# Performance work log

Measured on AMD Instinct MI355X. Metric: run time of the kernel, lower is better.

Reference implementation:

```python
import jax, jax.numpy as jnp
import numpy as np

D1, D2, DK, NH = 1024, 1024, 1024, 1
B, S = 4, 2048


def setup_inputs() -> dict:
    key = jax.random.key(0)
    ks = jax.random.split(key, 12)
    scale1 = 1.0 / np.sqrt(D1)
    scale2 = 1.0 / np.sqrt(D2)
    scalek = 1.0 / np.sqrt(DK)
    return {
        "x": jax.random.normal(ks[0], (B, S, D1), dtype=jnp.float32),
        "y": jax.random.normal(ks[1], (B, S, D2), dtype=jnp.float32),
        "adj": jax.random.uniform(ks[2], (B, S, S), dtype=jnp.float32),
        "Wq": jax.random.uniform(ks[3], (D1, DK), jnp.float32, -scale1, scale1),
        "bq": jax.random.uniform(ks[4], (DK,), jnp.float32, -scale1, scale1),
        "Wk": jax.random.uniform(ks[5], (D2, DK), jnp.float32, -scale2, scale2),
        "bk": jax.random.uniform(ks[6], (DK,), jnp.float32, -scale2, scale2),
        "Wv": jax.random.uniform(ks[7], (D2, DK), jnp.float32, -scale2, scale2),
        "bv": jax.random.uniform(ks[8], (DK,), jnp.float32, -scale2, scale2),
        "Wo": jax.random.uniform(ks[9], (DK, D2), jnp.float32, -scalek, scalek),
        "bo": jax.random.uniform(ks[10], (D2,), jnp.float32, -scalek, scalek),
    }


def reference(x, y, adj, Wq, bq, Wk, bk, Wv, bv, Wo, bo):
    # Single-head (n_heads=1) cross-attention with additive adjacency bias.
    dk_head = DK // NH
    norm = 1.0 / np.sqrt(DK)
    Q = (x @ Wq + bq).reshape(NH, B, S, dk_head)   # [h,b,s,d]
    K = (y @ Wk + bk).reshape(NH, B, S, dk_head)
    V = (y @ Wv + bv).reshape(NH, B, S, dk_head)
    att = jnp.einsum('hbsd,hbtd->hbst', Q, K) * norm  # [h,b,s,t]
    att = jax.nn.softmax(att + adj, axis=-1)          # adj [b,s,t] broadcasts over h
    tmp = jnp.einsum('hbst,hbtd->hbsd', att, V).reshape(B, S, -1)  # [b,s,dk]
    out = (tmp @ Wo + bo).reshape(-1, S, D2)
    return out
```

## Files before the change

### kernel.cpp

```cpp
#include <hip/hip_runtime.h>
#include <stdint.h>

typedef unsigned short u16;
using bf16x8 = __attribute__((ext_vector_type(8))) short;
using f32x4  = __attribute__((ext_vector_type(4))) float;

#define NORM 0.03125f

enum { M_PROJ = 0, M_EXP = 1, M_PV = 2, M_OUT = 3 };

__device__ __forceinline__ u16 f2bf(float f) {
  uint32_t u = __float_as_uint(f);
  return (u16)((u + 0x7FFFu + ((u >> 16) & 1u)) >> 16);
}

__device__ __forceinline__ void gload_lds16(const void* g, void* lds) {
  __builtin_amdgcn_global_load_lds(
      (const __attribute__((address_space(1))) uint32_t*)g,
      (__attribute__((address_space(3))) uint32_t*)lds, 16, 0, 0);
}

__global__ void k_cvt(const float* __restrict__ in, u16* __restrict__ out, int n4) {
  int i = blockIdx.x * blockDim.x + threadIdx.x;
  if (i >= n4) return;
  float4 v = ((const float4*)in)[i];
  uint32_t lo = f2bf(v.x) | ((uint32_t)f2bf(v.y) << 16);
  uint32_t hi = f2bf(v.z) | ((uint32_t)f2bf(v.w) << 16);
  ((uint2*)out)[i] = make_uint2(lo, hi);
}

__global__ void k_tc(const float* __restrict__ W0, const float* __restrict__ W1,
                     const float* __restrict__ W2, const float* __restrict__ W3,
                     u16* __restrict__ dst) {
  __shared__ float t[64][65];
  const float* W = blockIdx.z == 0 ? W0 : blockIdx.z == 1 ? W1 : blockIdx.z == 2 ? W2 : W3;
  u16* WT = dst + (size_t)blockIdx.z * (1024 * 1024);
  int c0 = blockIdx.x * 64, r0 = blockIdx.y * 64;
  int c = threadIdx.x & 63, q = threadIdx.x >> 6;
  for (int r = q; r < 64; r += 4) t[r][c] = W[(size_t)(r0 + r) * 1024 + c0 + c];
  __syncthreads();
  for (int r = q; r < 64; r += 4) WT[(size_t)(c0 + r) * 1024 + r0 + c] = f2bf(t[c][r]);
}

struct GArgs {
  const u16* A; const u16* B; int lda, ldb; long long bstrideB; int K;
  const float* bias; const float* adj; float* dpart; const float* dpart_r;
  void* C; int ldc;
  const u16* A1; const u16* B1; const u16* B2;
  const float* bias1; const float* bias2; void* C1; void* C2;
};

template <int MODE>
__global__ __launch_bounds__(512, 2) void gemm8(GArgs g) {
  __shared__ __align__(16) u16 sm[65536];

  const int tid = threadIdx.x, lane = tid & 63, wid = tid >> 6;
  const int wm = wid >> 2, wn = wid & 3;
  const int m0 = blockIdx.x * 256;
  const int n0 = blockIdx.y * 256;
  const int b = m0 >> 11;

  const u16* A = g.A; const u16* B = g.B;
  const float* bias = g.bias; void* C = g.C;
  int zmode = 0;
  if constexpr (MODE == M_PROJ) {
    int z = blockIdx.z; zmode = z;
    if (z == 1) { A = g.A1; B = g.B1; bias = g.bias1; C = g.C1; }
    else if (z == 2) { A = g.A1; B = g.B2; bias = g.bias2; C = g.C2; }
  }
  const int lda = g.lda, ldb = g.ldb, K = g.K, NT = K >> 6;
  const u16* Bp = B + (size_t)b * g.bstrideB;

  f32x4 acc[8][4] = {};

  auto stage = [&](const u16* src, int ld, int r0, int kc, int dst_u16) {
#pragma unroll
    for (int j = 0; j < 2; ++j) {
      int row = wid * 16 + j * 128 + (lane >> 2);
      int cb = (lane & 3) * 16;
      int csw = cb ^ ((row & 8) << 2);
      gload_lds16(src + (size_t)(r0 + row) * ld + kc + (csw >> 1),
                  (void*)&sm[dst_u16 + wid * 512 + j * 4096]);
    }
  };
  auto stA = [&](int v, int kh) {
    stage(A, lda, m0, v * 64 + kh * 32, (v & 1) * 32768 + kh * 8192);
  };
  auto stB = [&](int v, int kh) {
    stage(Bp, ldb, n0, v * 64 + kh * 32, (v & 1) * 32768 + 16384 + kh * 8192);
  };

  stA(0, 0); stB(0, 0); stA(0, 1); stB(0, 1);
  stA(1, 0); stB(1, 0);
  __builtin_amdgcn_sched_barrier(0);
  asm volatile("s_waitcnt vmcnt(8)" ::: "memory");
  __builtin_amdgcn_sched_barrier(0);
  __builtin_amdgcn_s_barrier();
  __builtin_amdgcn_sched_barrier(0);

  const int cb = (lane >> 4) * 16;
  for (int u = 0; u < NT; ++u) {
    const int base = (u & 1) * 32768;
#pragma unroll
    for (int ph = 0; ph < 4; ++ph) {
      const int h = ph & 1, kh = ph >> 1;
      bf16x8 af[4], bfr[4];
#pragma unroll
      for (int m = 0; m < 4; ++m) {
        int row = wm * 128 + h * 64 + m * 16 + (lane & 15);
        af[m] = *(const bf16x8*)__builtin_assume_aligned(
            &sm[base + kh * 8192 + row * 32 + ((cb ^ ((row & 8) << 2)) >> 1)], 16);
      }
#pragma unroll
      for (int n = 0; n < 4; ++n) {
        int row = wn * 64 + n * 16 + (lane & 15);
        bfr[n] = *(const bf16x8*)__builtin_assume_aligned(
            &sm[base + 16384 + kh * 8192 + row * 32 + ((cb ^ ((row & 8) << 2)) >> 1)], 16);
      }
      if (ph == 0) {
        if (u + 1 < NT) stA(u + 1, 1);
      } else if (ph == 1) {
        if (u + 1 < NT) stB(u + 1, 1);
        __builtin_amdgcn_sched_barrier(0);
        if (u + 1 < NT) asm volatile("s_waitcnt vmcnt(4)" ::: "memory");
        else            asm volatile("s_waitcnt vmcnt(0)" ::: "memory");
        __builtin_amdgcn_sched_barrier(0);
      } else if (ph == 2) {
        if (u + 2 < NT) stA(u + 2, 0);
      } else {
        if (u + 2 < NT) stB(u + 2, 0);
      }
      __builtin_amdgcn_s_barrier();
      __builtin_amdgcn_sched_barrier(0);
      __builtin_amdgcn_s_setprio(1);
#pragma unroll
      for (int m = 0; m < 4; ++m)
#pragma unroll
        for (int n = 0; n < 4; ++n)
          acc[h * 4 + m][n] = __builtin_amdgcn_mfma_f32_16x16x32_bf16(
              af[m], bfr[n], acc[h * 4 + m][n], 0, 0, 0);
      __builtin_amdgcn_s_setprio(0);
      __builtin_amdgcn_sched_barrier(0);
      asm volatile("s_waitcnt lgkmcnt(0)" ::: "memory");
      __builtin_amdgcn_sched_barrier(0);
      __builtin_amdgcn_s_barrier();
      __builtin_amdgcn_sched_barrier(0);
    }
  }

  const int lr = lane >> 4, lc = lane & 15;

  if constexpr (MODE == M_PROJ) {
    if (zmode < 2) {
      u16* Cc = (u16*)C;
#pragma unroll
      for (int i = 0; i < 8; ++i) {
        int rowo = (i >> 2) * 64 + (i & 3) * 16;
#pragma unroll
        for (int n = 0; n < 4; ++n) {
          int gcol = n0 + wn * 64 + n * 16 + lc;
          float bv = bias[gcol];
#pragma unroll
          for (int r = 0; r < 4; ++r) {
            int grow = m0 + wm * 128 + rowo + lr * 4 + r;
            Cc[(size_t)grow * g.ldc + gcol] = f2bf(acc[i][n][r] + bv);
          }
        }
      }
    } else {
      u16* Cc = (u16*)C;
#pragma unroll
      for (int i = 0; i < 8; ++i) {
        int rowo = (i >> 2) * 64 + (i & 3) * 16;
        int grow0 = m0 + wm * 128 + rowo + lr * 4;
        int t0 = grow0 & 2047;
#pragma unroll
        for (int n = 0; n < 4; ++n) {
          int gcol = n0 + wn * 64 + n * 16 + lc;
          float bv = bias[gcol];
          ushort4 pk = make_ushort4(f2bf(acc[i][n][0] + bv), f2bf(acc[i][n][1] + bv),
                                    f2bf(acc[i][n][2] + bv), f2bf(acc[i][n][3] + bv));
          *(ushort4*)&Cc[((size_t)b * 1024 + gcol) * 2048 + t0] = pk;
        }
      }
    }
  } else if constexpr (MODE == M_EXP) {
    u16* Cc = (u16*)C;
    float esum[8][4];
#pragma unroll
    for (int i = 0; i < 8; ++i)
#pragma unroll
      for (int r = 0; r < 4; ++r) esum[i][r] = 0.f;
#pragma unroll
    for (int i = 0; i < 8; ++i) {
      int rowo = (i >> 2) * 64 + (i & 3) * 16;
#pragma unroll
      for (int n = 0; n < 4; ++n) {
        int gcol = n0 + wn * 64 + n * 16 + lc;
#pragma unroll
        for (int r = 0; r < 4; ++r) {
          int grow = m0 + wm * 128 + rowo + lr * 4 + r;
          float z = acc[i][n][r] * NORM + g.adj[(size_t)grow * 2048 + gcol];
          float e = __expf(z);
          Cc[(size_t)grow * 2048 + gcol] = f2bf(e);
          esum[i][r] += e;
        }
      }
    }
    int pidx = blockIdx.y * 4 + wn;
#pragma unroll
    for (int i = 0; i < 8; ++i) {
      int rowo = (i >> 2) * 64 + (i & 3) * 16;
#pragma unroll
      for (int r = 0; r < 4; ++r) {
        float s = esum[i][r];
        s += __shfl_xor(s, 1); s += __shfl_xor(s, 2);
        s += __shfl_xor(s, 4); s += __shfl_xor(s, 8);
        if (lc == 0)
          g.dpart[(size_t)pidx * 8192 + m0 + wm * 128 + rowo + lr * 4 + r] = s;
      }
    }
  } else if constexpr (MODE == M_PV) {
    __shared__ float dinv[256];
    if (tid < 256) {
      float s = 0.f;
#pragma unroll
      for (int t = 0; t < 32; ++t) s += g.dpart_r[(size_t)t * 8192 + m0 + tid];
      dinv[tid] = 1.0f / s;
    }
    __syncthreads();
    u16* Cc = (u16*)C;
#pragma unroll
    for (int i = 0; i < 8; ++i) {
      int rowo = (i >> 2) * 64 + (i & 3) * 16;
#pragma unroll
      for (int n = 0; n < 4; ++n) {
        int gcol = n0 + wn * 64 + n * 16 + lc;
#pragma unroll
        for (int r = 0; r < 4; ++r) {
          int lrow = wm * 128 + rowo + lr * 4 + r;
          Cc[(size_t)(m0 + lrow) * g.ldc + gcol] = f2bf(acc[i][n][r] * dinv[lrow]);
        }
      }
    }
  } else {
    float* Cc = (float*)C;
#pragma unroll
    for (int i = 0; i < 8; ++i) {
      int rowo = (i >> 2) * 64 + (i & 3) * 16;
#pragma unroll
      for (int n = 0; n < 4; ++n) {
        int gcol = n0 + wn * 64 + n * 16 + lc;
        float bv = bias[gcol];
#pragma unroll
        for (int r = 0; r < 4; ++r) {
          int grow = m0 + wm * 128 + rowo + lr * 4 + r;
          Cc[(size_t)grow * g.ldc + gcol] = acc[i][n][r] + bv;
        }
      }
    }
  }
}

extern "C" void kernel_launch(void* const* d_in, const int* in_sizes, int n_in,
                              void* d_out, int out_size, void* d_ws, size_t ws_size,
                              hipStream_t stream) {
  const float* x   = (const float*)d_in[0];
  const float* y   = (const float*)d_in[1];
  const float* adj = (const float*)d_in[2];
  const float* Wq  = (const float*)d_in[3];
  const float* bq  = (const float*)d_in[4];
  const float* Wk  = (const float*)d_in[5];
  const float* bk  = (const float*)d_in[6];
  const float* Wv  = (const float*)d_in[7];
  const float* bv  = (const float*)d_in[8];
  const float* Wo  = (const float*)d_in[9];
  const float* bo  = (const float*)d_in[10];
  float* out = (float*)d_out;

  char* ws = (char*)d_ws;
  if (ws_size < 143654912ULL) return;
  u16* xb = (u16*)(ws);
  u16* yb = (u16*)(ws + 16777216);
  u16* WT = (u16*)(ws + 33554432);
  u16* Qb = (u16*)(ws + 41943040);
  u16* Kb = (u16*)(ws + 58720256);
  u16* Vt = (u16*)(ws + 75497472);
  u16* E  = (u16*)(ws + 92274688);
  float* dpart = (float*)(ws + 125829120);
  u16* tmpb = (u16*)(ws + 126877696);

  u16* WqT = WT;
  u16* WkT = WT + 1048576;
  u16* WvT = WT + 2097152;
  u16* WoT = WT + 3145728;

  k_cvt<<<8192, 256, 0, stream>>>(x, xb, 2097152);
  k_cvt<<<8192, 256, 0, stream>>>(y, yb, 2097152);
  k_tc<<<dim3(16, 16, 4), 256, 0, stream>>>(Wq, Wk, Wv, Wo, WT);

  GArgs ga;
  ga.A = xb; ga.B = WqT; ga.lda = 1024; ga.ldb = 1024; ga.bstrideB = 0; ga.K = 1024;
  ga.bias = bq; ga.adj = nullptr; ga.dpart = nullptr; ga.dpart_r = nullptr;
  ga.C = Qb; ga.ldc = 1024;
  ga.A1 = yb; ga.B1 = WkT; ga.B2 = WvT; ga.bias1 = bk; ga.bias2 = bv;
  ga.C1 = Kb; ga.C2 = Vt;
  gemm8<M_PROJ><<<dim3(32, 4, 3), 512, 0, stream>>>(ga);

  GArgs ge = {};
  ge.A = Qb; ge.B = Kb; ge.lda = 1024; ge.ldb = 1024; ge.bstrideB = 2097152LL; ge.K = 1024;
  ge.bias = nullptr; ge.adj = adj; ge.dpart = dpart; ge.dpart_r = nullptr;
  ge.C = E; ge.ldc = 2048;
  gemm8<M_EXP><<<dim3(32, 8), 512, 0, stream>>>(ge);

  GArgs gp = {};
  gp.A = E; gp.B = Vt; gp.lda = 2048; gp.ldb = 2048; gp.bstrideB = 2097152LL; gp.K = 2048;
  gp.bias = nullptr; gp.adj = nullptr; gp.dpart = nullptr; gp.dpart_r = dpart;
  gp.C = tmpb; gp.ldc = 1024;
  gemm8<M_PV><<<dim3(32, 4), 512, 0, stream>>>(gp);

  GArgs go = {};
  go.A = tmpb; go.B = WoT; go.lda = 1024; go.ldb = 1024; go.bstrideB = 0; go.K = 1024;
  go.bias = bo; go.adj = nullptr; go.dpart = nullptr; go.dpart_r = nullptr;
  go.C = out; go.ldc = 1024;
  gemm8<M_OUT><<<dim3(32, 4), 512, 0, stream>>>(go);
}
```

Measured before the change: 266.7 us.

## Shrink GEMM M-tile to 128 and use triple-buffered LDS pipeline

```diff
diff --git a/kernel.cpp b/kernel.cpp
--- a/kernel.cpp
+++ b/kernel.cpp
@@ -51,12 +51,12 @@
 };
 
 template <int MODE>
-__global__ __launch_bounds__(512, 2) void gemm8(GArgs g) {
-  __shared__ __align__(16) u16 sm[65536];
+__global__ __launch_bounds__(512, 2) void gemm3(GArgs g) {
+  __shared__ __align__(16) u16 sm[73728];
 
   const int tid = threadIdx.x, lane = tid & 63, wid = tid >> 6;
   const int wm = wid >> 2, wn = wid & 3;
-  const int m0 = blockIdx.x * 256;
+  const int m0 = blockIdx.x * 128;
   const int n0 = blockIdx.y * 256;
   const int b = m0 >> 11;
 
@@ -71,81 +71,75 @@
   const int lda = g.lda, ldb = g.ldb, K = g.K, NT = K >> 6;
   const u16* Bp = B + (size_t)b * g.bstrideB;
 
-  f32x4 acc[8][4] = {};
-
-  auto stage = [&](const u16* src, int ld, int r0, int kc, int dst_u16) {
+  f32x4 acc[4][4] = {};
+
+  const int srow = tid >> 2;
+  const int scb = (tid & 3) * 16;
+  auto stageA = [&](int v, int kh, int bufb) {
+    int csw = scb ^ ((srow & 8) << 2);
+    gload_lds16(A + (size_t)(m0 + srow) * lda + v * 64 + kh * 32 + (csw >> 1),
+                (void*)&sm[bufb + kh * 4096 + srow * 32 + (tid & 3) * 8]);
+  };
+  auto stageB = [&](int v, int kh, int bufb) {
 #pragma unroll
     for (int j = 0; j < 2; ++j) {
-      int row = wid * 16 + j * 128 + (lane >> 2);
-      int cb = (lane & 3) * 16;
-      int csw = cb ^ ((row & 8) << 2);
-      gload_lds16(src + (size_t)(r0 + row) * ld + kc + (csw >> 1),
-                  (void*)&sm[dst_u16 + wid * 512 + j * 4096]);
+      int row = j * 128 + srow;
+      int csw = scb ^ ((row & 8) << 2);
+      gload_lds16(Bp + (size_t)(n0 + row) * ldb + v * 64 + kh * 32 + (csw >> 1),
+                  (void*)&sm[bufb + 8192 + kh * 8192 + row * 32 + (tid & 3) * 8]);
     }
   };
-  auto stA = [&](int v, int kh) {
-    stage(A, lda, m0, v * 64 + kh * 32, (v & 1) * 32768 + kh * 8192);
-  };
-  auto stB = [&](int v, int kh) {
-    stage(Bp, ldb, n0, v * 64 + kh * 32, (v & 1) * 32768 + 16384 + kh * 8192);
-  };
-
-  stA(0, 0); stB(0, 0); stA(0, 1); stB(0, 1);
-  stA(1, 0); stB(1, 0);
-  __builtin_amdgcn_sched_barrier(0);
-  asm volatile("s_waitcnt vmcnt(8)" ::: "memory");
-  __builtin_amdgcn_sched_barrier(0);
+
+  stageA(0, 0, 0);     stageB(0, 0, 0);
+  stageA(0, 1, 0);     stageB(0, 1, 0);
+  stageA(1, 0, 24576); stageB(1, 0, 24576);
+  stageA(1, 1, 24576); stageB(1, 1, 24576);
+  asm volatile("s_waitcnt vmcnt(9)" ::: "memory");
   __builtin_amdgcn_s_barrier();
-  __builtin_amdgcn_sched_barrier(0);
 
   const int cb = (lane >> 4) * 16;
+  const int fr = lane & 15;
+  int rd = 0;
   for (int u = 0; u < NT; ++u) {
-    const int base = (u & 1) * 32768;
-#pragma unroll
-    for (int ph = 0; ph < 4; ++ph) {
-      const int h = ph & 1, kh = ph >> 1;
+    const int bufb = rd * 24576;
+    const int stb = (rd == 0 ? 2 : rd - 1) * 24576;
+#pragma unroll
+    for (int kh = 0; kh < 2; ++kh) {
       bf16x8 af[4], bfr[4];
 #pragma unroll
       for (int m = 0; m < 4; ++m) {
-        int row = wm * 128 + h * 64 + m * 16 + (lane & 15);
+        int row = wm * 64 + m * 16 + fr;
         af[m] = *(const bf16x8*)__builtin_assume_aligned(
-            &sm[base + kh * 8192 + row * 32 + ((cb ^ ((row & 8) << 2)) >> 1)], 16);
+            &sm[bufb + kh * 4096 + row * 32 + ((cb ^ ((row & 8) << 2)) >> 1)], 16);
       }
 #pragma unroll
       for (int n = 0; n < 4; ++n) {
-        int row = wn * 64 + n * 16 + (lane & 15);
+        int row = wn * 64 + n * 16 + fr;
         bfr[n] = *(const bf16x8*)__builtin_assume_aligned(
-            &sm[base + 16384 + kh * 8192 + row * 32 + ((cb ^ ((row & 8) << 2)) >> 1)], 16);
-      }
-      if (ph == 0) {
-        if (u + 1 < NT) stA(u + 1, 1);
-      } else if (ph == 1) {
-        if (u + 1 < NT) stB(u + 1, 1);
-        __builtin_amdgcn_sched_barrier(0);
-        if (u + 1 < NT) asm volatile("s_waitcnt vmcnt(4)" ::: "memory");
-        else            asm volatile("s_waitcnt vmcnt(0)" ::: "memory");
-        __builtin_amdgcn_sched_barrier(0);
-      } else if (ph == 2) {
-        if (u + 2 < NT) stA(u + 2, 0);
+            &sm[bufb + 8192 + kh * 8192 + row * 32 + ((cb ^ ((row & 8) << 2)) >> 1)], 16);
+      }
+      if (u + 2 < NT) {
+        stageA(u + 2, kh, stb);
+        stageB(u + 2, kh, stb);
+        asm volatile("s_waitcnt vmcnt(9)" ::: "memory");
+      } else if (kh == 0) {
+        if (u == NT - 2) asm volatile("s_waitcnt vmcnt(6)" ::: "memory");
+        else             asm volatile("s_waitcnt vmcnt(0)" ::: "memory");
       } else {
-        if (u + 2 < NT) stB(u + 2, 0);
+        if (u == NT - 2) asm volatile("s_waitcnt vmcnt(3)" ::: "memory");
       }
       __builtin_amdgcn_s_barrier();
-      __builtin_amdgcn_sched_barrier(0);
       __builtin_amdgcn_s_setprio(1);
 #pragma unroll
       for (int m = 0; m < 4; ++m)
 #pragma unroll
         for (int n = 0; n < 4; ++n)
-          acc[h * 4 + m][n] = __builtin_amdgcn_mfma_f32_16x16x32_bf16(
-              af[m], bfr[n], acc[h * 4 + m][n], 0, 0, 0);
+          acc[m][n] = __builtin_amdgcn_mfma_f32_16x16x32_bf16(
+              af[m], bfr[n], acc[m][n], 0, 0, 0);
       __builtin_amdgcn_s_setprio(0);
-      __builtin_amdgcn_sched_barrier(0);
-      asm volatile("s_waitcnt lgkmcnt(0)" ::: "memory");
-      __builtin_amdgcn_sched_barrier(0);
       __builtin_amdgcn_s_barrier();
-      __builtin_amdgcn_sched_barrier(0);
     }
+    rd = (rd == 2) ? 0 : rd + 1;
   }
 
   const int lr = lane >> 4, lc = lane & 15;
@@ -154,75 +148,68 @@
     if (zmode < 2) {
       u16* Cc = (u16*)C;
 #pragma unroll
-      for (int i = 0; i < 8; ++i) {
-        int rowo = (i >> 2) * 64 + (i & 3) * 16;
+      for (int m = 0; m < 4; ++m)
 #pragma unroll
         for (int n = 0; n < 4; ++n) {
           int gcol = n0 + wn * 64 + n * 16 + lc;
           float bv = bias[gcol];
 #pragma unroll
           for (int r = 0; r < 4; ++r) {
-            int grow = m0 + wm * 128 + rowo + lr * 4 + r;
-            Cc[(size_t)grow * g.ldc + gcol] = f2bf(acc[i][n][r] + bv);
+            int grow = m0 + wm * 64 + m * 16 + lr * 4 + r;
+            Cc[(size_t)grow * g.ldc + gcol] = f2bf(acc[m][n][r] + bv);
           }
         }
-      }
     } else {
       u16* Cc = (u16*)C;
 #pragma unroll
-      for (int i = 0; i < 8; ++i) {
-        int rowo = (i >> 2) * 64 + (i & 3) * 16;
-        int grow0 = m0 + wm * 128 + rowo + lr * 4;
+      for (int m = 0; m < 4; ++m) {
+        int grow0 = m0 + wm * 64 + m * 16 + lr * 4;
         int t0 = grow0 & 2047;
 #pragma unroll
         for (int n = 0; n < 4; ++n) {
           int gcol = n0 + wn * 64 + n * 16 + lc;
           float bv = bias[gcol];
-          ushort4 pk = make_ushort4(f2bf(acc[i][n][0] + bv), f2bf(acc[i][n][1] + bv),
-                                    f2bf(acc[i][n][2] + bv), f2bf(acc[i][n][3] + bv));
+          ushort4 pk = make_ushort4(f2bf(acc[m][n][0] + bv), f2bf(acc[m][n][1] + bv),
+                                    f2bf(acc[m][n][2] + bv), f2bf(acc[m][n][3] + bv));
           *(ushort4*)&Cc[((size_t)b * 1024 + gcol) * 2048 + t0] = pk;
         }
       }
     }
   } else if constexpr (MODE == M_EXP) {
     u16* Cc = (u16*)C;
-    float esum[8][4];
-#pragma unroll
-    for (int i = 0; i < 8; ++i)
-#pragma unroll
-      for (int r = 0; r < 4; ++r) esum[i][r] = 0.f;
-#pragma unroll
-    for (int i = 0; i < 8; ++i) {
-      int rowo = (i >> 2) * 64 + (i & 3) * 16;
+    float esum[4][4];
+#pragma unroll
+    for (int m = 0; m < 4; ++m)
+#pragma unroll
+      for (int r = 0; r < 4; ++r) esum[m][r] = 0.f;
+#pragma unroll
+    for (int m = 0; m < 4; ++m)
 #pragma unroll
       for (int n = 0; n < 4; ++n) {
         int gcol = n0 + wn * 64 + n * 16 + lc;
 #pragma unroll
         for (int r = 0; r < 4; ++r) {
-          int grow = m0 + wm * 128 + rowo + lr * 4 + r;
-          float z = acc[i][n][r] * NORM + g.adj[(size_t)grow * 2048 + gcol];
+          int grow = m0 + wm * 64 + m * 16 + lr * 4 + r;
+          float z = acc[m][n][r] * NORM + g.adj[(size_t)grow * 2048 + gcol];
           float e = __expf(z);
           Cc[(size_t)grow * 2048 + gcol] = f2bf(e);
-          esum[i][r] += e;
-        }
-      }
-    }
+          esum[m][r] += e;
+        }
+      }
     int pidx = blockIdx.y * 4 + wn;
 #pragma unroll
-    for (int i = 0; i < 8; ++i) {
-      int rowo = (i >> 2) * 64 + (i & 3) * 16;
+    for (int m = 0; m < 4; ++m)
 #pragma unroll
       for (int r = 0; r < 4; ++r) {
-        float s = esum[i][r];
+        float s = esum[m][r];
         s += __shfl_xor(s, 1); s += __shfl_xor(s, 2);
         s += __shfl_xor(s, 4); s += __shfl_xor(s, 8);
         if (lc == 0)
-          g.dpart[(size_t)pidx * 8192 + m0 + wm * 128 + rowo + lr * 4 + r] = s;
-      }
-    }
+          g.dpart[(size_t)pidx * 8192 + m0 + wm * 64 + m * 16 + lr * 4 + r] = s;
+      }
   } else if constexpr (MODE == M_PV) {
-    __shared__ float dinv[256];
-    if (tid < 256) {
+    __shared__ float dinv[128];
+    if (tid < 128) {
       float s = 0.f;
 #pragma unroll
       for (int t = 0; t < 32; ++t) s += g.dpart_r[(size_t)t * 8192 + m0 + tid];
@@ -231,34 +218,30 @@
     __syncthreads();
     u16* Cc = (u16*)C;
 #pragma unroll
-    for (int i = 0; i < 8; ++i) {
-      int rowo = (i >> 2) * 64 + (i & 3) * 16;
+    for (int m = 0; m < 4; ++m)
 #pragma unroll
       for (int n = 0; n < 4; ++n) {
         int gcol = n0 + wn * 64 + n * 16 + lc;
 #pragma unroll
         for (int r = 0; r < 4; ++r) {
-          int lrow = wm * 128 + rowo + lr * 4 + r;
-          Cc[(size_t)(m0 + lrow) * g.ldc + gcol] = f2bf(acc[i][n][r] * dinv[lrow]);
-        }
-      }
-    }
+          int lrow = wm * 64 + m * 16 + lr * 4 + r;
+          Cc[(size_t)(m0 + lrow) * g.ldc + gcol] = f2bf(acc[m][n][r] * dinv[lrow]);
+        }
+      }
   } else {
     float* Cc = (float*)C;
 #pragma unroll
-    for (int i = 0; i < 8; ++i) {
-      int rowo = (i >> 2) * 64 + (i & 3) * 16;
+    for (int m = 0; m < 4; ++m)
 #pragma unroll
       for (int n = 0; n < 4; ++n) {
         int gcol = n0 + wn * 64 + n * 16 + lc;
         float bv = bias[gcol];
 #pragma unroll
         for (int r = 0; r < 4; ++r) {
-          int grow = m0 + wm * 128 + rowo + lr * 4 + r;
-          Cc[(size_t)grow * g.ldc + gcol] = acc[i][n][r] + bv;
-        }
-      }
-    }
+          int grow = m0 + wm * 64 + m * 16 + lr * 4 + r;
+          Cc[(size_t)grow * g.ldc + gcol] = acc[m][n][r] + bv;
+        }
+      }
   }
 }
 
@@ -305,23 +288,23 @@
   ga.C = Qb; ga.ldc = 1024;
   ga.A1 = yb; ga.B1 = WkT; ga.B2 = WvT; ga.bias1 = bk; ga.bias2 = bv;
   ga.C1 = Kb; ga.C2 = Vt;
-  gemm8<M_PROJ><<<dim3(32, 4, 3), 512, 0, stream>>>(ga);
+  gemm3<M_PROJ><<<dim3(64, 4, 3), 512, 0, stream>>>(ga);
 
   GArgs ge = {};
   ge.A = Qb; ge.B = Kb; ge.lda = 1024; ge.ldb = 1024; ge.bstrideB = 2097152LL; ge.K = 1024;
   ge.bias = nullptr; ge.adj = adj; ge.dpart = dpart; ge.dpart_r = nullptr;
   ge.C = E; ge.ldc = 2048;
-  gemm8<M_EXP><<<dim3(32, 8), 512, 0, stream>>>(ge);
+  gemm3<M_EXP><<<dim3(64, 8), 512, 0, stream>>>(ge);
 
   GArgs gp = {};
   gp.A = E; gp.B = Vt; gp.lda = 2048; gp.ldb = 2048; gp.bstrideB = 2097152LL; gp.K = 2048;
   gp.bias = nullptr; gp.adj = nullptr; gp.dpart = nullptr; gp.dpart_r = dpart;
   gp.C = tmpb; gp.ldc = 1024;
-  gemm8<M_PV><<<dim3(32, 4), 512, 0, stream>>>(gp);
+  gemm3<M_PV><<<dim3(64, 4), 512, 0, stream>>>(gp);
 
   GArgs go = {};
   go.A = tmpb; go.B = WoT; go.lda = 1024; go.ldb = 1024; go.bstrideB = 0; go.K = 1024;
   go.bias = bo; go.adj = nullptr; go.dpart = nullptr; go.dpart_r = nullptr;
   go.C = out; go.ldc = 1024;
-  gemm8<M_OUT><<<dim3(32, 4), 512, 0, stream>>>(go);
-}
+  gemm3<M_OUT><<<dim3(64, 4), 512, 0, stream>>>(go);
+}
```

After: 234.7 us. -12.0%, faster.

## Restructure GEMM main loop with 64-wide K tiles and XCD-aware block remap

Applied to the files above, without the earlier changes.

```diff
diff --git a/kernel.cpp b/kernel.cpp
--- a/kernel.cpp
+++ b/kernel.cpp
@@ -51,13 +51,25 @@
 };
 
 template <int MODE>
-__global__ __launch_bounds__(512, 2) void gemm8(GArgs g) {
+__global__ __launch_bounds__(512, 2) void gemm4(GArgs g) {
   __shared__ __align__(16) u16 sm[65536];
+  __shared__ float dinv[256];
 
   const int tid = threadIdx.x, lane = tid & 63, wid = tid >> 6;
   const int wm = wid >> 2, wn = wid & 3;
-  const int m0 = blockIdx.x * 256;
-  const int n0 = blockIdx.y * 256;
+
+  int bx = blockIdx.x, by = blockIdx.y;
+  if constexpr (MODE == M_EXP) {
+    int L = bx + (by << 5), xcd = L & 7, j = L >> 3;
+    bx = ((xcd & 3) << 3) + (j & 7);
+    by = ((xcd >> 2) << 2) + (j >> 3);
+  } else if constexpr (MODE == M_PV) {
+    int L = bx + (by << 5), xcd = L & 7, j = L >> 3;
+    bx = ((xcd & 3) << 3) + (j & 7);
+    by = ((xcd >> 2) << 1) + (j >> 3);
+  }
+  const int m0 = bx * 256;
+  const int n0 = by * 256;
   const int b = m0 >> 11;
 
   const u16* A = g.A; const u16* B = g.B;
@@ -73,80 +85,94 @@
 
   f32x4 acc[8][4] = {};
 
-  auto stage = [&](const u16* src, int ld, int r0, int kc, int dst_u16) {
-#pragma unroll
-    for (int j = 0; j < 2; ++j) {
-      int row = wid * 16 + j * 128 + (lane >> 2);
-      int cb = (lane & 3) * 16;
-      int csw = cb ^ ((row & 8) << 2);
-      gload_lds16(src + (size_t)(r0 + row) * ld + kc + (csw >> 1),
-                  (void*)&sm[dst_u16 + wid * 512 + j * 4096]);
+  auto stA = [&](int v, int q, int sb) {
+#pragma unroll
+    for (int l = 0; l < 2; ++l) {
+      int sr = l * 64 + (tid >> 3);
+      int grow = m0 + ((sr >> 6) << 7) + (q << 6) + (sr & 63);
+      int csrc = ((tid & 7) * 8) ^ ((sr & 7) << 3);
+      gload_lds16(A + (size_t)grow * lda + v * 64 + csrc,
+                  (void*)&sm[sb + q * 8192 + l * 4096 + tid * 8]);
     }
   };
-  auto stA = [&](int v, int kh) {
-    stage(A, lda, m0, v * 64 + kh * 32, (v & 1) * 32768 + kh * 8192);
+  auto stB = [&](int v, int h, int sb) {
+#pragma unroll
+    for (int l = 0; l < 2; ++l) {
+      int sr = h * 128 + l * 64 + (tid >> 3);
+      int csrc = ((tid & 7) * 8) ^ ((sr & 7) << 3);
+      gload_lds16(Bp + (size_t)(n0 + sr) * ldb + v * 64 + csrc,
+                  (void*)&sm[sb + 16384 + h * 8192 + l * 4096 + tid * 8]);
+    }
   };
-  auto stB = [&](int v, int kh) {
-    stage(Bp, ldb, n0, v * 64 + kh * 32, (v & 1) * 32768 + 16384 + kh * 8192);
-  };
-
-  stA(0, 0); stB(0, 0); stA(0, 1); stB(0, 1);
-  stA(1, 0); stB(1, 0);
-  __builtin_amdgcn_sched_barrier(0);
+
+  stB(0, 0, 0); stB(0, 1, 0); stA(0, 0, 0);
+  stA(0, 1, 0);
+  stB(1, 0, 32768); stB(1, 1, 32768); stA(1, 0, 32768);
   asm volatile("s_waitcnt vmcnt(8)" ::: "memory");
-  __builtin_amdgcn_sched_barrier(0);
   __builtin_amdgcn_s_barrier();
-  __builtin_amdgcn_sched_barrier(0);
-
-  const int cb = (lane >> 4) * 16;
+
+  const int fr = lane & 15, hi = lane >> 4;
+  const int swz = (fr & 7) << 3;
+  const int awb = wm * 64;
+  const int bwb = wn * 64;
+
+  bf16x8 af[4], bfr[4];
+
+#define RD_A(q, ks)                                                         \
+  _Pragma("unroll") for (int m = 0; m < 4; ++m) {                           \
+    int sr = awb + m * 16 + fr;                                             \
+    af[m] = *(const bf16x8*)__builtin_assume_aligned(                       \
+        &sm[dbase + (q) * 8192 + sr * 64 + (((ks) * 32 + hi * 8) ^ swz)], 16); \
+  }
+#define RD_B(ks)                                                            \
+  _Pragma("unroll") for (int n = 0; n < 4; ++n) {                           \
+    int sr = bwb + n * 16 + fr;                                             \
+    bfr[n] = *(const bf16x8*)__builtin_assume_aligned(                      \
+        &sm[dbase + 16384 + sr * 64 + (((ks) * 32 + hi * 8) ^ swz)], 16);   \
+  }
+#define MFMA_Q(q)                                                           \
+  __builtin_amdgcn_s_setprio(1);                                            \
+  _Pragma("unroll") for (int m = 0; m < 4; ++m)                             \
+  _Pragma("unroll") for (int n = 0; n < 4; ++n)                             \
+      acc[(q) * 4 + m][n] = __builtin_amdgcn_mfma_f32_16x16x32_bf16(        \
+          af[m], bfr[n], acc[(q) * 4 + m][n], 0, 0, 0);                     \
+  __builtin_amdgcn_s_setprio(0);
+
   for (int u = 0; u < NT; ++u) {
-    const int base = (u & 1) * 32768;
-#pragma unroll
-    for (int ph = 0; ph < 4; ++ph) {
-      const int h = ph & 1, kh = ph >> 1;
-      bf16x8 af[4], bfr[4];
-#pragma unroll
-      for (int m = 0; m < 4; ++m) {
-        int row = wm * 128 + h * 64 + m * 16 + (lane & 15);
-        af[m] = *(const bf16x8*)__builtin_assume_aligned(
-            &sm[base + kh * 8192 + row * 32 + ((cb ^ ((row & 8) << 2)) >> 1)], 16);
-      }
-#pragma unroll
-      for (int n = 0; n < 4; ++n) {
-        int row = wn * 64 + n * 16 + (lane & 15);
-        bfr[n] = *(const bf16x8*)__builtin_assume_aligned(
-            &sm[base + 16384 + kh * 8192 + row * 32 + ((cb ^ ((row & 8) << 2)) >> 1)], 16);
-      }
-      if (ph == 0) {
-        if (u + 1 < NT) stA(u + 1, 1);
-      } else if (ph == 1) {
-        if (u + 1 < NT) stB(u + 1, 1);
-        __builtin_amdgcn_sched_barrier(0);
-        if (u + 1 < NT) asm volatile("s_waitcnt vmcnt(4)" ::: "memory");
-        else            asm volatile("s_waitcnt vmcnt(0)" ::: "memory");
-        __builtin_amdgcn_sched_barrier(0);
-      } else if (ph == 2) {
-        if (u + 2 < NT) stA(u + 2, 0);
-      } else {
-        if (u + 2 < NT) stB(u + 2, 0);
-      }
-      __builtin_amdgcn_s_barrier();
-      __builtin_amdgcn_sched_barrier(0);
-      __builtin_amdgcn_s_setprio(1);
-#pragma unroll
-      for (int m = 0; m < 4; ++m)
-#pragma unroll
-        for (int n = 0; n < 4; ++n)
-          acc[h * 4 + m][n] = __builtin_amdgcn_mfma_f32_16x16x32_bf16(
-              af[m], bfr[n], acc[h * 4 + m][n], 0, 0, 0);
-      __builtin_amdgcn_s_setprio(0);
-      __builtin_amdgcn_sched_barrier(0);
-      asm volatile("s_waitcnt lgkmcnt(0)" ::: "memory");
-      __builtin_amdgcn_sched_barrier(0);
-      __builtin_amdgcn_s_barrier();
-      __builtin_amdgcn_sched_barrier(0);
-    }
-  }
+    const int dbase = (u & 1) << 15;
+    const int sbase = dbase ^ 32768;
+
+    RD_B(0); RD_A(0, 0);
+    if (u + 1 < NT) stA(u + 1, 1, sbase);
+    __builtin_amdgcn_s_barrier();
+    MFMA_Q(0);
+    if (u + 1 < NT) asm volatile("s_waitcnt vmcnt(8)" ::: "memory");
+    else            asm volatile("s_waitcnt vmcnt(0)" ::: "memory");
+    __builtin_amdgcn_s_barrier();
+
+    RD_A(1, 0);
+    __builtin_amdgcn_s_barrier();
+    MFMA_Q(1);
+    __builtin_amdgcn_s_barrier();
+
+    RD_B(1); RD_A(0, 1);
+    __builtin_amdgcn_s_barrier();
+    MFMA_Q(0);
+    __builtin_amdgcn_s_barrier();
+
+    RD_A(1, 1);
+    if (u + 2 < NT) { stB(u + 2, 0, dbase); stB(u + 2, 1, dbase); stA(u + 2, 0, dbase); }
+    __builtin_amdgcn_s_barrier();
+    MFMA_Q(1);
+    if (u + 1 < NT) {
+      if (u + 2 < NT) asm volatile("s_waitcnt vmcnt(8)" ::: "memory");
+      else            asm volatile("s_waitcnt vmcnt(2)" ::: "memory");
+    }
+    __builtin_amdgcn_s_barrier();
+  }
+#undef RD_A
+#undef RD_B
+#undef MFMA_Q
 
   const int lr = lane >> 4, lc = lane & 15;
 
@@ -207,7 +233,7 @@
         }
       }
     }
-    int pidx = blockIdx.y * 4 + wn;
+    int pidx = by * 4 + wn;
 #pragma unroll
     for (int i = 0; i < 8; ++i) {
       int rowo = (i >> 2) * 64 + (i & 3) * 16;
@@ -221,7 +247,6 @@
       }
     }
   } else if constexpr (MODE == M_PV) {
-    __shared__ float dinv[256];
     if (tid < 256) {
       float s = 0.f;
 #pragma unroll
@@ -305,23 +330,23 @@
   ga.C = Qb; ga.ldc = 1024;
   ga.A1 = yb; ga.B1 = WkT; ga.B2 = WvT; ga.bias1 = bk; ga.bias2 = bv;
   ga.C1 = Kb; ga.C2 = Vt;
-  gemm8<M_PROJ><<<dim3(32, 4, 3), 512, 0, stream>>>(ga);
+  gemm4<M_PROJ><<<dim3(32, 4, 3), 512, 0, stream>>>(ga);
 
   GArgs ge = {};
   ge.A = Qb; ge.B = Kb; ge.lda = 1024; ge.ldb = 1024; ge.bstrideB = 2097152LL; ge.K = 1024;
   ge.bias = nullptr; ge.adj = adj; ge.dpart = dpart; ge.dpart_r = nullptr;
   ge.C = E; ge.ldc = 2048;
-  gemm8<M_EXP><<<dim3(32, 8), 512, 0, stream>>>(ge);
+  gemm4<M_EXP><<<dim3(32, 8), 512, 0, stream>>>(ge);
 
   GArgs gp = {};
   gp.A = E; gp.B = Vt; gp.lda = 2048; gp.ldb = 2048; gp.bstrideB = 2097152LL; gp.K = 2048;
   gp.bias = nullptr; gp.adj = nullptr; gp.dpart = nullptr; gp.dpart_r = dpart;
   gp.C = tmpb; gp.ldc = 1024;
-  gemm8<M_PV><<<dim3(32, 4), 512, 0, stream>>>(gp);
+  gemm4<M_PV><<<dim3(32, 4), 512, 0, stream>>>(gp);
 
   GArgs go = {};
   go.A = tmpb; go.B = WoT; go.lda = 1024; go.ldb = 1024; go.bstrideB = 0; go.K = 1024;
   go.bias = bo; go.adj = nullptr; go.dpart = nullptr; go.dpart_r = nullptr;
   go.C = out; go.ldc = 1024;
-  gemm8<M_OUT><<<dim3(32, 4), 512, 0, stream>>>(go);
-}
+  gemm4<M_OUT><<<dim3(32, 4), 512, 0, stream>>>(go);
+}
```

Result: slower. 275.0 us (+3.1%).
